# Optimization experiments

Measured on AMD Instinct MI355X. Metric: run time of the kernel, lower is better.

Reference implementation:

```python
import jax, jax.numpy as jnp
import numpy as np

B_, L_, H_, D_, N_, R_, K_ = 2, 1024, 2048, 4096, 16, 128, 4


def setup_inputs() -> dict:
    key = jax.random.key(0)
    ks = jax.random.split(key, 8)
    s = lambda k, shp, sc: jax.random.normal(k, shp, jnp.float32) * sc
    x = s(ks[0], (B_, L_, H_), 1.0)
    in_proj_w = s(ks[1], (2 * D_, H_), 0.02)
    conv_w = s(ks[2], (D_, 1, K_), 0.1)          # depthwise conv kernel (OIW, I=1)
    conv_b = s(ks[3], (D_,), 0.02)
    x_proj_w = s(ks[4], (R_ + 2 * N_, D_), 0.02)
    dt_proj_w = s(ks[5], (D_, R_), 0.02)
    dt_proj_b = s(ks[6], (D_,), 0.02)
    # A_log init as in module: log(arange(1..N)) expanded over channels
    A_log = jnp.log(jnp.broadcast_to(jnp.arange(1, N_ + 1, dtype=jnp.float32), (D_, N_)))
    D = jnp.ones((D_,), jnp.float32)
    out_proj_w = s(ks[7], (H_, D_), 0.02)
    return dict(x=x, in_proj_w=in_proj_w, conv_w=conv_w, conv_b=conv_b,
                x_proj_w=x_proj_w, dt_proj_w=dt_proj_w, dt_proj_b=dt_proj_b,
                A_log=A_log, D=D, out_proj_w=out_proj_w)


def reference(x, in_proj_w, conv_w, conv_b, x_proj_w, dt_proj_w, dt_proj_b, A_log, D, out_proj_w):
    Bsz, L, H = x.shape
    # in_proj -> split into ssm branch and gate branch
    proj = x @ in_proj_w.T                               # [B, L, 2D]
    h, gate = jnp.split(proj, 2, axis=-1)                # each [B, L, D]
    # causal depthwise conv1d over time (left pad K-1, truncate to L)
    hc = h.transpose(0, 2, 1)                            # [B, D, L]
    conv = jax.lax.conv_general_dilated(
        hc, conv_w, window_strides=(1,), padding=[(K_ - 1, 0)],
        dimension_numbers=('NCW', 'OIW', 'NCW'), feature_group_count=hc.shape[1])
    u = jax.nn.silu(conv + conv_b[None, :, None]).transpose(0, 2, 1)  # [B, L, D]
    # input-dependent SSM parameters
    ssm_p = u @ x_proj_w.T                               # [B, L, R+2N]
    dt, Bm, Cm = jnp.split(ssm_p, [R_, R_ + N_], axis=-1)
    dt = jax.nn.softplus(dt @ dt_proj_w.T + dt_proj_b)   # [B, L, D]
    A = -jnp.exp(A_log)                                  # [D, N]

    def step(state, inp):
        dt_t, B_t, C_t, u_t = inp                        # [B,D],[B,N],[B,N],[B,D]
        dA = jnp.exp(dt_t[:, :, None] * A)               # [B, D, N]
        dBu = dt_t[:, :, None] * B_t[:, None, :] * u_t[:, :, None]
        state = state * dA + dBu                         # [B, D, N]
        y = jnp.einsum('bdn,bn->bd', state, C_t)
        return state, y

    init = jnp.zeros((Bsz, u.shape[-1], N_), x.dtype)
    _, ys = jax.lax.scan(step, init, (dt.transpose(1, 0, 2), Bm.transpose(1, 0, 2),
                                      Cm.transpose(1, 0, 2), u.transpose(1, 0, 2)))
    y = ys.transpose(1, 0, 2)                            # [B, L, D]
    y = (y + u * D) * jax.nn.silu(gate)
    return y @ out_proj_w.T                              # [B, L, H]
```

## Files before the change

kernel.cpp:

```cpp
#include <hip/hip_runtime.h>
#include <hip/hip_bf16.h>
#include <cstdint>
#include <cstddef>

typedef __hip_bfloat16 bf16;
typedef __attribute__((ext_vector_type(8))) short short8;
typedef __attribute__((ext_vector_type(4))) float f32x4;

#define BB 2
#define LL 1024
#define HH 2048
#define DD 4096
#define NN 16
#define RR 128
#define KK 4
#define TT (BB*LL)
#define NC 16
#define LC (LL/NC)
#define KSPLIT 8

__device__ __forceinline__ void gload_lds16(const void* g, void* l) {
  __builtin_amdgcn_global_load_lds(
      (__attribute__((address_space(1))) void*)(g),
      (__attribute__((address_space(3))) void*)(l), 16, 0, 0);
}

__global__ void probe_dtype(const unsigned int* __restrict__ alog, int* __restrict__ flag) {
  if (threadIdx.x == 0 && blockIdx.x == 0) *flag = (alog[0] != 0u) ? 1 : 0;
}

__global__ __launch_bounds__(256) void cvt_bf16(
    const void* __restrict__ src, bf16* __restrict__ dst,
    int n4, const int* __restrict__ flag)
{
  const bool isb = (*flag != 0);
  const int stride = gridDim.x * blockDim.x;
  for (int i = blockIdx.x * blockDim.x + threadIdx.x; i < n4; i += stride) {
    if (isb) {
      ((uint2*)dst)[i] = ((const uint2*)src)[i];
    } else {
      float4 v = ((const float4*)src)[i];
      dst[i*4+0] = __float2bfloat16(v.x);
      dst[i*4+1] = __float2bfloat16(v.y);
      dst[i*4+2] = __float2bfloat16(v.z);
      dst[i*4+3] = __float2bfloat16(v.w);
    }
  }
}

template<int EPI>
__global__ __launch_bounds__(256) void gemm_bt(
    const bf16* __restrict__ A, const bf16* __restrict__ Bw,
    bf16* __restrict__ Cb, float* __restrict__ Cf,
    const void* __restrict__ bias,
    int M, int N, int K, int ldk, int Nvalid, const int* __restrict__ flag)
{
  __shared__ __align__(16) short As[3*128*32];
  __shared__ __align__(16) short Bs[3*128*32];
  const int tid = threadIdx.x;
  const int w = tid >> 6, l = tid & 63;
  const int lr = l & 15, lk = l >> 4;
  const int m0 = blockIdx.x * 128, n0 = blockIdx.y * 128;
  const int wm = (w >> 1) * 64, wn = (w & 1) * 64;

  f32x4 acc[4][4] = {};

  const int sr0 = (w*2+0)*16 + (l>>2);
  const int sr1 = (w*2+1)*16 + (l>>2);
  const int sc0 = (((l&3) ^ ((sr0>>1)&3)) << 3);
  const int sc1 = (((l&3) ^ ((sr1>>1)&3)) << 3);
  const int lo0 = (w*2+0)*512 + l*8;
  const int lo1 = (w*2+1)*512 + l*8;

  const size_t arow0 = (size_t)(m0 + sr0);
  const size_t arow1 = (size_t)(m0 + sr1);
  const size_t brow0 = (size_t)min(n0 + sr0, N-1);
  const size_t brow1 = (size_t)min(n0 + sr1, N-1);
  const size_t kb = (size_t)blockIdx.z * K;

  const int NT = K >> 5;

  auto stage = [&](int t) {
    const int s = t % 3;
    const size_t ko = kb + (size_t)(t << 5);
    gload_lds16(A  + arow0*ldk + ko + sc0, &As[s*4096 + lo0]);
    gload_lds16(A  + arow1*ldk + ko + sc1, &As[s*4096 + lo1]);
    gload_lds16(Bw + brow0*ldk + ko + sc0, &Bs[s*4096 + lo0]);
    gload_lds16(Bw + brow1*ldk + ko + sc1, &Bs[s*4096 + lo1]);
  };

  stage(0);
  stage(1);
  asm volatile("s_waitcnt vmcnt(4)" ::: "memory");
  __builtin_amdgcn_s_barrier();

  for (int t = 0; t < NT; ++t) {
    if (t + 2 < NT) stage(t + 2);
    const int s = t % 3;
    short8 a[4], b[4];
#pragma unroll
    for (int m = 0; m < 4; m++) {
      const int row = wm + m*16 + lr;
      a[m] = *(const short8*)&As[s*4096 + row*32 + ((lk ^ ((row>>1)&3)) << 3)];
    }
#pragma unroll
    for (int n = 0; n < 4; n++) {
      const int row = wn + n*16 + lr;
      b[n] = *(const short8*)&Bs[s*4096 + row*32 + ((lk ^ ((row>>1)&3)) << 3)];
    }
#pragma unroll
    for (int m = 0; m < 4; m++)
#pragma unroll
      for (int n = 0; n < 4; n++)
        acc[m][n] = __builtin_amdgcn_mfma_f32_16x16x32_bf16(a[m], b[n], acc[m][n], 0, 0, 0);

    if (t + 2 < NT) {
      asm volatile("s_waitcnt vmcnt(4)" ::: "memory");
      __builtin_amdgcn_s_barrier();
    } else if (t + 1 < NT) {
      asm volatile("s_waitcnt vmcnt(0)" ::: "memory");
      __builtin_amdgcn_s_barrier();
    }
  }

  bool isb = false;
  if constexpr (EPI == 1 || EPI == 3) isb = (*flag != 0);

#pragma unroll
  for (int m = 0; m < 4; m++) {
#pragma unroll
    for (int n = 0; n < 4; n++) {
#pragma unroll
      for (int r = 0; r < 4; r++) {
        const int row = m0 + wm + m*16 + lk*4 + r;
        const int col = n0 + wn + n*16 + lr;
        float v = acc[m][n][r];
        if constexpr (EPI == 0) {
          Cb[(size_t)row*N + col] = __float2bfloat16(v);
        } else if constexpr (EPI == 1) {
          const float bv = isb ? __bfloat162float(((const bf16*)bias)[col])
                               : ((const float*)bias)[col];
          v += bv;
          v = fmaxf(v, 0.f) + log1pf(expf(-fabsf(v)));
          Cb[(size_t)row*N + col] = __float2bfloat16(v);
        } else if constexpr (EPI == 3) {
          if (isb) Cb[(size_t)row*N + col] = __float2bfloat16(v);
          else     Cf[(size_t)row*N + col] = v;
        } else {
          if (col < Nvalid)
            Cf[(size_t)blockIdx.z*M*Nvalid + (size_t)row*Nvalid + col] = v;
        }
      }
    }
  }
}

__global__ __launch_bounds__(256) void reduce_ssm(
    const float* __restrict__ part, float* __restrict__ ssm,
    bf16* __restrict__ dtin)
{
  const int id = blockIdx.x*256 + threadIdx.x;
  const int row = id / 160, col = id - row*160;
  float v = 0.f;
#pragma unroll
  for (int s = 0; s < KSPLIT; s++) v += part[(size_t)s*TT*160 + id];
  ssm[id] = v;
  if (col < 128) dtin[(size_t)row*128 + col] = __float2bfloat16(v);
}

__global__ __launch_bounds__(256) void conv_silu(
    const bf16* __restrict__ proj, const void* __restrict__ cw,
    const void* __restrict__ cb, bf16* __restrict__ u,
    const int* __restrict__ flag)
{
  const int d  = blockIdx.x * 256 + threadIdx.x;
  const int t0 = blockIdx.y * 64;
  const int l0 = t0 & (LL-1);
  const bool isb = (*flag != 0);
  float w0, w1, w2, w3, bv;
  if (isb) {
    const bf16* c = (const bf16*)cw;
    w0 = __bfloat162float(c[d*KK+0]); w1 = __bfloat162float(c[d*KK+1]);
    w2 = __bfloat162float(c[d*KK+2]); w3 = __bfloat162float(c[d*KK+3]);
    bv = __bfloat162float(((const bf16*)cb)[d]);
  } else {
    const float* c = (const float*)cw;
    w0 = c[d*KK+0]; w1 = c[d*KK+1]; w2 = c[d*KK+2]; w3 = c[d*KK+3];
    bv = ((const float*)cb)[d];
  }
  float hm3 = 0.f, hm2 = 0.f, hm1 = 0.f;
  if (l0 > 0) {
    hm3 = __bfloat162float(proj[(size_t)(t0-3)*(2*DD) + d]);
    hm2 = __bfloat162float(proj[(size_t)(t0-2)*(2*DD) + d]);
    hm1 = __bfloat162float(proj[(size_t)(t0-1)*(2*DD) + d]);
  }
  for (int i = 0; i < 64; i++) {
    const int t = t0 + i;
    const float hc = __bfloat162float(proj[(size_t)t*(2*DD) + d]);
    const float a = bv + w0*hm3 + w1*hm2 + w2*hm1 + w3*hc;
    const float s = a / (1.f + __expf(-a));
    u[(size_t)t*DD + d] = __float2bfloat16(s);
    hm3 = hm2; hm2 = hm1; hm1 = hc;
  }
}

__global__ __launch_bounds__(256) void scan_pass1(
    const bf16* __restrict__ dt, const bf16* __restrict__ u,
    const float* __restrict__ ssm, const void* __restrict__ Alog,
    float* __restrict__ dtsum, float* __restrict__ Sb,
    const int* __restrict__ flag)
{
  const int d = blockIdx.x * 256 + threadIdx.x;
  const int c = blockIdx.y, b = blockIdx.z;
  const bool isb = (*flag != 0);
  float Av[NN];
#pragma unroll
  for (int n = 0; n < NN; n++) {
    const float alv = isb ? __bfloat162float(((const bf16*)Alog)[d*NN + n])
                          : ((const float*)Alog)[d*NN + n];
    Av[n] = -__expf(alv);
  }
  float st[NN];
#pragma unroll
  for (int n = 0; n < NN; n++) st[n] = 0.f;
  float dsum = 0.f;
  const size_t tok0 = (size_t)b * LL + (size_t)c * LC;

  float dtv = __bfloat162float(dt[tok0*DD + d]);
  float uv  = __bfloat162float(u [tok0*DD + d]);
  float4 Bp0 = *(const float4*)&ssm[tok0*160 + RR];
  float4 Bp1 = *(const float4*)&ssm[tok0*160 + RR + 4];
  float4 Bp2 = *(const float4*)&ssm[tok0*160 + RR + 8];
  float4 Bp3 = *(const float4*)&ssm[tok0*160 + RR + 12];

  for (int i = 0; i < LC; i++) {
    const float dtc = dtv, uc = uv;
    const float Bv[NN] = {Bp0.x,Bp0.y,Bp0.z,Bp0.w, Bp1.x,Bp1.y,Bp1.z,Bp1.w,
                          Bp2.x,Bp2.y,Bp2.z,Bp2.w, Bp3.x,Bp3.y,Bp3.z,Bp3.w};
    if (i < LC-1) {
      const size_t tk = tok0 + i + 1;
      dtv = __bfloat162float(dt[tk*DD + d]);
      uv  = __bfloat162float(u [tk*DD + d]);
      Bp0 = *(const float4*)&ssm[tk*160 + RR];
      Bp1 = *(const float4*)&ssm[tk*160 + RR + 4];
      Bp2 = *(const float4*)&ssm[tk*160 + RR + 8];
      Bp3 = *(const float4*)&ssm[tk*160 + RR + 12];
    }
    const float dtu = dtc * uc;
    dsum += dtc;
#pragma unroll
    for (int n = 0; n < NN; n++) {
      const float dA = __expf(dtc * Av[n]);
      st[n] = fmaf(st[n], dA, Bv[n] * dtu);
    }
  }
  dtsum[((size_t)b*NC + c)*DD + d] = dsum;
  float4* Sp = (float4*)&Sb[(((size_t)b*NC + c)*DD + d)*NN];
  Sp[0] = make_float4(st[0],  st[1],  st[2],  st[3]);
  Sp[1] = make_float4(st[4],  st[5],  st[6],  st[7]);
  Sp[2] = make_float4(st[8],  st[9],  st[10], st[11]);
  Sp[3] = make_float4(st[12], st[13], st[14], st[15]);
}

__global__ __launch_bounds__(256) void scan_pass2(
    const float* __restrict__ dtsum, float* __restrict__ Sb,
    const void* __restrict__ Alog, const int* __restrict__ flag)
{
  const int id = blockIdx.x * 256 + threadIdx.x;
  const int b = id >> 16;
  const int r = id & (DD*NN - 1);
  const int d = r >> 4, n = r & 15;
  const bool isb = (*flag != 0);
  const float alv = isb ? __bfloat162float(((const bf16*)Alog)[d*NN + n])
                        : ((const float*)Alog)[d*NN + n];
  const float Av = -__expf(alv);
  float carry = 0.f;
  size_t sidx = (size_t)b * NC * DD * NN + r;
  size_t didx = (size_t)b * NC * DD + d;
#pragma unroll
  for (int c = 0; c < NC; c++) {
    const float p = __expf(Av * dtsum[didx]);
    const float s = Sb[sidx];
    Sb[sidx] = carry;
    carry = p * carry + s;
    sidx += (size_t)DD * NN;
    didx += (size_t)DD;
  }
}

__global__ __launch_bounds__(256) void scan_pass3(
    const bf16* __restrict__ dt, const bf16* __restrict__ u,
    const float* __restrict__ ssm, const bf16* __restrict__ proj,
    const void* __restrict__ Alog, const void* __restrict__ Dp,
    const float* __restrict__ Sb,
    bf16* __restrict__ yout, const int* __restrict__ flag)
{
  const int d = blockIdx.x * 256 + threadIdx.x;
  const int c = blockIdx.y, b = blockIdx.z;
  const bool isb = (*flag != 0);
  float Av[NN];
#pragma unroll
  for (int n = 0; n < NN; n++) {
    const float alv = isb ? __bfloat162float(((const bf16*)Alog)[d*NN + n])
                          : ((const float*)Alog)[d*NN + n];
    Av[n] = -__expf(alv);
  }
  const float Dval = isb ? __bfloat162float(((const bf16*)Dp)[d])
                         : ((const float*)Dp)[d];
  float st[NN];
  {
    const float4* Sp = (const float4*)&Sb[(((size_t)b*NC + c)*DD + d)*NN];
    float4 s0 = Sp[0], s1 = Sp[1], s2 = Sp[2], s3 = Sp[3];
    st[0]=s0.x; st[1]=s0.y; st[2]=s0.z; st[3]=s0.w;
    st[4]=s1.x; st[5]=s1.y; st[6]=s1.z; st[7]=s1.w;
    st[8]=s2.x; st[9]=s2.y; st[10]=s2.z; st[11]=s2.w;
    st[12]=s3.x; st[13]=s3.y; st[14]=s3.z; st[15]=s3.w;
  }
  const size_t tok0 = (size_t)b * LL + (size_t)c * LC;

  float dtv = __bfloat162float(dt[tok0*DD + d]);
  float uv  = __bfloat162float(u [tok0*DD + d]);
  float gv  = __bfloat162float(proj[tok0*(2*DD) + DD + d]);
  float4 Bp0 = *(const float4*)&ssm[tok0*160 + RR];
  float4 Bp1 = *(const float4*)&ssm[tok0*160 + RR + 4];
  float4 Bp2 = *(const float4*)&ssm[tok0*160 + RR + 8];
  float4 Bp3 = *(const float4*)&ssm[tok0*160 + RR + 12];
  float4 Cp0 = *(const float4*)&ssm[tok0*160 + RR + NN];
  float4 Cp1 = *(const float4*)&ssm[tok0*160 + RR + NN + 4];
  float4 Cp2 = *(const float4*)&ssm[tok0*160 + RR + NN + 8];
  float4 Cp3 = *(const float4*)&ssm[tok0*160 + RR + NN + 12];

  for (int i = 0; i < LC; i++) {
    const float dtc = dtv, uc = uv, gc = gv;
    const float Bv[NN] = {Bp0.x,Bp0.y,Bp0.z,Bp0.w, Bp1.x,Bp1.y,Bp1.z,Bp1.w,
                          Bp2.x,Bp2.y,Bp2.z,Bp2.w, Bp3.x,Bp3.y,Bp3.z,Bp3.w};
    const float Cv[NN] = {Cp0.x,Cp0.y,Cp0.z,Cp0.w, Cp1.x,Cp1.y,Cp1.z,Cp1.w,
                          Cp2.x,Cp2.y,Cp2.z,Cp2.w, Cp3.x,Cp3.y,Cp3.z,Cp3.w};
    if (i < LC-1) {
      const size_t tk = tok0 + i + 1;
      dtv = __bfloat162float(dt[tk*DD + d]);
      uv  = __bfloat162float(u [tk*DD + d]);
      gv  = __bfloat162float(proj[tk*(2*DD) + DD + d]);
      Bp0 = *(const float4*)&ssm[tk*160 + RR];
      Bp1 = *(const float4*)&ssm[tk*160 + RR + 4];
      Bp2 = *(const float4*)&ssm[tk*160 + RR + 8];
      Bp3 = *(const float4*)&ssm[tk*160 + RR + 12];
      Cp0 = *(const float4*)&ssm[tk*160 + RR + NN];
      Cp1 = *(const float4*)&ssm[tk*160 + RR + NN + 4];
      Cp2 = *(const float4*)&ssm[tk*160 + RR + NN + 8];
      Cp3 = *(const float4*)&ssm[tk*160 + RR + NN + 12];
    }
    const float dtu = dtc * uc;
    float y = uc * Dval;
#pragma unroll
    for (int n = 0; n < NN; n++) {
      const float dA = __expf(dtc * Av[n]);
      st[n] = fmaf(st[n], dA, Bv[n] * dtu);
      y = fmaf(st[n], Cv[n], y);
    }
    const float sg = gc / (1.f + __expf(-gc));
    yout[(tok0 + i)*DD + d] = __float2bfloat16(y * sg);
  }
}

extern "C" void kernel_launch(void* const* d_in, const int* in_sizes, int n_in,
                              void* d_out, int out_size, void* d_ws, size_t ws_size,
                              hipStream_t stream)
{
  const void* x    = d_in[0];
  const void* wIn  = d_in[1];
  const void* cw   = d_in[2];
  const void* cb   = d_in[3];
  const void* xw   = d_in[4];
  const void* dtw  = d_in[5];
  const void* dtb  = d_in[6];
  const void* Alog = d_in[7];
  const void* Dp   = d_in[8];
  const void* ow   = d_in[9];

  char* ws = (char*)d_ws;
  bf16*  proj  = (bf16*) (ws + 0);
  bf16*  u     = (bf16*) (ws + 33554432);
  float* ssm   = (float*)(ws + 50331648);
  bf16*  dtin  = (bf16*) (ws + 51642368);
  bf16*  dtbuf = (bf16*) (ws + 52166656);
  bf16*  yfin  = (bf16*) (ws + 68943872);
  bf16*  xb    = (bf16*) (ws + 52166656);
  bf16*  wInb  = (bf16*) (ws + 60555264);
  float* part  = (float*)(ws + 52166656);
  bf16*  owb   = (bf16*) (ws + 52166656);
  float* dtsum = (float*)(ws + 51642368);
  float* Sbuf  = (float*)(ws + 85721088);
  bf16*  xwb   = (bf16*) (ws + 94109696);
  bf16*  dtwb  = (bf16*) (ws + 95420416);
  int*   flag  = (int*)  (ws + 96468992);

  probe_dtype<<<1, 64, 0, stream>>>((const unsigned int*)Alog, flag);
  cvt_bf16<<<1024, 256, 0, stream>>>(x,   xb,   (BB*LL*HH)/4,   flag);
  cvt_bf16<<<1024, 256, 0, stream>>>(wIn, wInb, (2*DD*HH)/4,    flag);
  cvt_bf16<<<256,  256, 0, stream>>>(xw,  xwb,  ((RR+2*NN)*DD)/4, flag);
  cvt_bf16<<<256,  256, 0, stream>>>(dtw, dtwb, (DD*RR)/4,      flag);

  gemm_bt<0><<<dim3(TT/128, (2*DD)/128), 256, 0, stream>>>(
      xb, wInb, proj, nullptr, nullptr, TT, 2*DD, HH, HH, 2*DD, flag);
  conv_silu<<<dim3(DD/256, TT/64), 256, 0, stream>>>(proj, cw, cb, u, flag);
  gemm_bt<4><<<dim3(TT/128, 2, KSPLIT), 256, 0, stream>>>(
      u, xwb, nullptr, part, nullptr, TT, RR + 2*NN, DD/KSPLIT, DD, RR + 2*NN, flag);
  reduce_ssm<<<dim3(TT*160/256), 256, 0, stream>>>(part, ssm, dtin);
  gemm_bt<1><<<dim3(TT/128, DD/128), 256, 0, stream>>>(
      dtin, dtwb, dtbuf, nullptr, dtb, TT, DD, RR, RR, DD, flag);
  scan_pass1<<<dim3(DD/256, NC, BB), 256, 0, stream>>>(
      dtbuf, u, ssm, Alog, dtsum, Sbuf, flag);
  scan_pass2<<<dim3(BB*DD*NN/256), 256, 0, stream>>>(dtsum, Sbuf, Alog, flag);
  scan_pass3<<<dim3(DD/256, NC, BB), 256, 0, stream>>>(
      dtbuf, u, ssm, proj, Alog, Dp, Sbuf, yfin, flag);
  cvt_bf16<<<1024, 256, 0, stream>>>(ow, owb, (HH*DD)/4, flag);
  gemm_bt<3><<<dim3(TT/128, HH/128), 256, 0, stream>>>(
      yfin, owb, (bf16*)d_out, (float*)d_out, nullptr, TT, HH, DD, DD, HH, flag);
}
```

Baseline: 381.7 us.

## Use 256x256 tile GEMM for in_proj and split-K out_proj with reduction

Adds a 512-thread GEMM kernel with 256x256 tiles, a 64-deep K step and double-buffered LDS loads. It replaces the 128x128 kernel for the in_proj GEMM, which gives more data reuse per block. The out_proj GEMM now uses the same kernel split three ways over K (21/21/22 steps of 64), which fills more CUs since only 64 output tiles exist. A separate reduce kernel sums the partials and writes bf16 or fp32 output, at the cost of extra fp32 partial traffic through the workspace.

```diff
diff --git a/kernel.cpp b/kernel.cpp
--- a/kernel.cpp
+++ b/kernel.cpp
@@ -49,6 +49,131 @@
 }
 
 template<int EPI>
+__global__ __launch_bounds__(512, 1) void gemm256(
+    const bf16* __restrict__ A, const bf16* __restrict__ Bw,
+    bf16* __restrict__ Cb, float* __restrict__ Cf,
+    int M, int N, int K, int ldk)
+{
+  __shared__ __align__(16) short As[2*256*64];
+  __shared__ __align__(16) short Bs[2*256*64];
+  const int tid = threadIdx.x;
+  const int w = tid >> 6, l = tid & 63;
+  const int lr = l & 15, lk = l >> 4;
+  const int wr = w >> 2, wc = w & 3;
+  const int m0 = blockIdx.x * 256, n0 = blockIdx.y * 256;
+
+  int kofs = 0, nt = K >> 6;
+  if constexpr (EPI == 5) {
+    const int z = blockIdx.z;
+    kofs = z * 1344;
+    nt = (z == 2) ? 22 : 21;
+  }
+
+  const int srow = w*8 + (l>>3);
+  const int scol = (((l&7) ^ (l>>3)) << 3);
+  const int sld  = srow*64 + (l&7)*8;
+
+  f32x4 acc[8][4] = {};
+
+  const bf16* Ab = A  + (size_t)m0 * ldk + kofs;
+  const bf16* Bb = Bw + (size_t)n0 * ldk + kofs;
+
+  auto stage = [&](int t) {
+    const int buf = (t & 1) * 16384;
+    const size_t kk = (size_t)(t << 6);
+#pragma unroll
+    for (int i = 0; i < 4; i++)
+      gload_lds16(Ab + (size_t)(i*64 + srow) * ldk + kk + scol, &As[buf + i*4096 + sld]);
+#pragma unroll
+    for (int i = 0; i < 4; i++)
+      gload_lds16(Bb + (size_t)(i*64 + srow) * ldk + kk + scol, &Bs[buf + i*4096 + sld]);
+  };
+
+  stage(0);
+  stage(1);
+  asm volatile("s_waitcnt vmcnt(8)" ::: "memory");
+  __builtin_amdgcn_s_barrier();
+
+  for (int t = 0; t < nt; ++t) {
+    const int buf = (t & 1) * 16384;
+    short8 bfr[4][2];
+#pragma unroll
+    for (int nf = 0; nf < 4; nf++) {
+      const int r = wc*64 + nf*16 + lr;
+#pragma unroll
+      for (int ks = 0; ks < 2; ks++)
+        bfr[nf][ks] = *(const short8*)&Bs[buf + r*64 + (((ks*4+lk) ^ (r&7)) << 3)];
+    }
+#pragma unroll
+    for (int q = 0; q < 4; q++) {
+      short8 afr[2][2];
+#pragma unroll
+      for (int mi = 0; mi < 2; mi++) {
+        const int r = wr*128 + (q*2+mi)*16 + lr;
+#pragma unroll
+        for (int ks = 0; ks < 2; ks++)
+          afr[mi][ks] = *(const short8*)&As[buf + r*64 + (((ks*4+lk) ^ (r&7)) << 3)];
+      }
+#pragma unroll
+      for (int mi = 0; mi < 2; mi++)
+#pragma unroll
+        for (int nf = 0; nf < 4; nf++)
+#pragma unroll
+          for (int ks = 0; ks < 2; ks++)
+            acc[q*2+mi][nf] = __builtin_amdgcn_mfma_f32_16x16x32_bf16(
+                afr[mi][ks], bfr[nf][ks], acc[q*2+mi][nf], 0, 0, 0);
+    }
+    if (t + 1 < nt) {
+      asm volatile("" ::: "memory");
+      __builtin_amdgcn_s_barrier();
+      if (t + 2 < nt) {
+        stage(t + 2);
+        asm volatile("s_waitcnt vmcnt(8)" ::: "memory");
+      } else {
+        asm volatile("s_waitcnt vmcnt(0)" ::: "memory");
+      }
+      __builtin_amdgcn_s_barrier();
+    }
+  }
+
+#pragma unroll
+  for (int mf = 0; mf < 8; mf++)
+#pragma unroll
+    for (int nf = 0; nf < 4; nf++)
+#pragma unroll
+      for (int r = 0; r < 4; r++) {
+        const int row = m0 + wr*128 + mf*16 + lk*4 + r;
+        const int col = n0 + wc*64 + nf*16 + lr;
+        const float v = acc[mf][nf][r];
+        if constexpr (EPI == 0) {
+          Cb[(size_t)row*N + col] = __float2bfloat16(v);
+        } else {
+          Cf[(size_t)blockIdx.z*M*N + (size_t)row*N + col] = v;
+        }
+      }
+}
+
+__global__ __launch_bounds__(256) void reduce_out(
+    const float* __restrict__ part, bf16* __restrict__ ob, float* __restrict__ of,
+    const int* __restrict__ flag)
+{
+  const int id = blockIdx.x*256 + threadIdx.x;
+  const bool isb = (*flag != 0);
+  float4 a = ((const float4*)part)[id];
+  const float4 b = ((const float4*)(part + (size_t)TT*HH))[id];
+  const float4 c = ((const float4*)(part + (size_t)2*TT*HH))[id];
+  a.x += b.x + c.x; a.y += b.y + c.y; a.z += b.z + c.z; a.w += b.w + c.w;
+  if (isb) {
+    ob[id*4+0] = __float2bfloat16(a.x);
+    ob[id*4+1] = __float2bfloat16(a.y);
+    ob[id*4+2] = __float2bfloat16(a.z);
+    ob[id*4+3] = __float2bfloat16(a.w);
+  } else {
+    ((float4*)of)[id] = a;
+  }
+}
+
+template<int EPI>
 __global__ __launch_bounds__(256) void gemm_bt(
     const bf16* __restrict__ A, const bf16* __restrict__ Bw,
     bf16* __restrict__ Cb, float* __restrict__ Cf,
@@ -124,7 +249,7 @@
   }
 
   bool isb = false;
-  if constexpr (EPI == 1 || EPI == 3) isb = (*flag != 0);
+  if constexpr (EPI == 1) isb = (*flag != 0);
 
 #pragma unroll
   for (int m = 0; m < 4; m++) {
@@ -135,17 +260,12 @@
         const int row = m0 + wm + m*16 + lk*4 + r;
         const int col = n0 + wn + n*16 + lr;
         float v = acc[m][n][r];
-        if constexpr (EPI == 0) {
-          Cb[(size_t)row*N + col] = __float2bfloat16(v);
-        } else if constexpr (EPI == 1) {
+        if constexpr (EPI == 1) {
           const float bv = isb ? __bfloat162float(((const bf16*)bias)[col])
                                : ((const float*)bias)[col];
           v += bv;
           v = fmaxf(v, 0.f) + log1pf(expf(-fabsf(v)));
           Cb[(size_t)row*N + col] = __float2bfloat16(v);
-        } else if constexpr (EPI == 3) {
-          if (isb) Cb[(size_t)row*N + col] = __float2bfloat16(v);
-          else     Cf[(size_t)row*N + col] = v;
         } else {
           if (col < Nvalid)
             Cf[(size_t)blockIdx.z*M*Nvalid + (size_t)row*Nvalid + col] = v;
@@ -389,6 +509,7 @@
   bf16*  wInb  = (bf16*) (ws + 60555264);
   float* part  = (float*)(ws + 52166656);
   bf16*  owb   = (bf16*) (ws + 52166656);
+  float* part6 = (float*)(ws + 0);
   float* dtsum = (float*)(ws + 51642368);
   float* Sbuf  = (float*)(ws + 85721088);
   bf16*  xwb   = (bf16*) (ws + 94109696);
@@ -401,8 +522,8 @@
   cvt_bf16<<<256,  256, 0, stream>>>(xw,  xwb,  ((RR+2*NN)*DD)/4, flag);
   cvt_bf16<<<256,  256, 0, stream>>>(dtw, dtwb, (DD*RR)/4,      flag);
 
-  gemm_bt<0><<<dim3(TT/128, (2*DD)/128), 256, 0, stream>>>(
-      xb, wInb, proj, nullptr, nullptr, TT, 2*DD, HH, HH, 2*DD, flag);
+  gemm256<0><<<dim3(TT/256, (2*DD)/256), 512, 0, stream>>>(
+      xb, wInb, proj, nullptr, TT, 2*DD, HH, HH);
   conv_silu<<<dim3(DD/256, TT/64), 256, 0, stream>>>(proj, cw, cb, u, flag);
   gemm_bt<4><<<dim3(TT/128, 2, KSPLIT), 256, 0, stream>>>(
       u, xwb, nullptr, part, nullptr, TT, RR + 2*NN, DD/KSPLIT, DD, RR + 2*NN, flag);
@@ -415,6 +536,8 @@
   scan_pass3<<<dim3(DD/256, NC, BB), 256, 0, stream>>>(
       dtbuf, u, ssm, proj, Alog, Dp, Sbuf, yfin, flag);
   cvt_bf16<<<1024, 256, 0, stream>>>(ow, owb, (HH*DD)/4, flag);
-  gemm_bt<3><<<dim3(TT/128, HH/128), 256, 0, stream>>>(
-      yfin, owb, (bf16*)d_out, (float*)d_out, nullptr, TT, HH, DD, DD, HH, flag);
-}
+  gemm256<5><<<dim3(TT/256, HH/256, 3), 512, 0, stream>>>(
+      yfin, owb, nullptr, part6, TT, HH, 0, DD);
+  reduce_out<<<dim3(TT*HH/4/256), 256, 0, stream>>>(
+      part6, (bf16*)d_out, (float*)d_out, flag);
+}
```

Measured after the change: 321.4 us. -15.8%, faster.
